# Kernel optimization log

Hardware: AMD Instinct MI355X
Metric: run time of the kernel (lower is better)

## Reference

```python
import jax, jax.numpy as jnp
import numpy as np

B, S, H = 8, 2048, 1024

def setup_inputs() -> dict:
    key = jax.random.key(0)
    k1, k2 = jax.random.split(key)
    inputs = jax.random.normal(k1, (B, S, H), dtype=jnp.float32)
    # PyTorch Linear weight [out, in]; init ~ U(-1/sqrt(H), 1/sqrt(H)) approximated with scaled normal
    W = jax.random.normal(k2, (H, H), dtype=jnp.float32) * (1.0 / np.sqrt(H))
    b = jnp.zeros((H,), dtype=jnp.float32)
    return {"inputs": inputs, "W": W, "b": b}

def reference(inputs, W, b):
    # QW = inputs @ W^T + b   (nn.Linear)
    QW = jnp.einsum('bsh,oh->bso', inputs, W) + b  # [B,S,H]
    # score = QW @ inputs^T  (no scaling, no mask)
    score = jnp.einsum('bqh,bkh->bqk', QW, inputs)  # [B,S,S]
    attn = jax.nn.softmax(score, axis=2)
    # output = attn @ inputs
    output = jnp.einsum('bqk,bkh->bqh', attn, inputs)  # [B,S,H]
    return output
```

## Files before the change

kernel.cpp:

```cpp
#include <hip/hip_runtime.h>
#include <hip/hip_bf16.h>
#include <hip/hip_fp16.h>

typedef unsigned short u16;
typedef __attribute__((ext_vector_type(8))) _Float16 f16x8;
typedef __attribute__((ext_vector_type(4))) float f32x4;

#define B_ 8
#define S_ 2048
#define H_ 1024
#define M_ (B_ * S_)

__device__ __forceinline__ u16 f2h(float f) {
  _Float16 h = (_Float16)f;
  return __builtin_bit_cast(u16, h);
}

__global__ void f32_to_f16_kernel(const float* __restrict__ x,
                                  u16* __restrict__ o, int n4) {
  int stride = gridDim.x * blockDim.x;
  for (int i = blockIdx.x * blockDim.x + threadIdx.x; i < n4; i += stride) {
    float4 v = reinterpret_cast<const float4*>(x)[i];
    ushort4 h;
    h.x = f2h(v.x); h.y = f2h(v.y); h.z = f2h(v.z); h.w = f2h(v.w);
    reinterpret_cast<ushort4*>(o)[i] = h;
  }
}

__global__ __launch_bounds__(256) void transpose_f32_kernel(
    const float* __restrict__ x, u16* __restrict__ xt, u16* __restrict__ xf) {
  __shared__ u16 t[64][72];
  int b = blockIdx.z, s0 = blockIdx.x * 64, h0 = blockIdx.y * 64;
  int tid = threadIdx.x;
  int row = tid & 63, seg = tid >> 6;
  const float* src = x + ((size_t)(b * S_ + s0 + row)) * H_ + h0 + seg * 16;
  u16* dstf = xf + ((size_t)(b * S_ + s0 + row)) * H_ + h0 + seg * 16;
#pragma unroll
  for (int j = 0; j < 4; ++j) {
    float4 v = reinterpret_cast<const float4*>(src)[j];
    ushort4 h;
    h.x = f2h(v.x); h.y = f2h(v.y); h.z = f2h(v.z); h.w = f2h(v.w);
    reinterpret_cast<ushort4*>(dstf)[j] = h;
    *reinterpret_cast<ushort4*>(&t[row][seg * 16 + j * 4]) = h;
  }
  __syncthreads();
  int hh = tid & 63, ss = tid >> 6;
  u16* dst = xt + ((size_t)(b * H_ + h0 + hh)) * S_ + s0 + ss * 16;
#pragma unroll
  for (int j = 0; j < 4; ++j) {
    ushort4 o;
    o.x = t[ss * 16 + j * 4 + 0][hh];
    o.y = t[ss * 16 + j * 4 + 1][hh];
    o.z = t[ss * 16 + j * 4 + 2][hh];
    o.w = t[ss * 16 + j * 4 + 3][hh];
    reinterpret_cast<ushort4*>(dst)[j] = o;
  }
}

__device__ __forceinline__ void async_stage16(const u16* g, u16* l) {
  __builtin_amdgcn_global_load_lds(
      (__attribute__((address_space(1))) void*)g,
      (__attribute__((address_space(3))) void*)l, 16, 0, 0);
}

template <int OM>
__global__ __launch_bounds__(512) void gemm8_kernel(
    const u16* __restrict__ A, const u16* __restrict__ B,
    float* __restrict__ Cf, u16* __restrict__ Ch,
    const float* __restrict__ bias,
    int lda, int ldb, int ldc, int K,
    long sAz, long sBz, long sCz) {
  __shared__ __align__(16) u16 sA[2][256 * 64];
  __shared__ __align__(16) u16 sB[2][256 * 64];

  int gx = gridDim.x, gy = gridDim.y;
  int nwg = gx * gy * gridDim.z;
  int wgid = blockIdx.x + gx * (blockIdx.y + gy * blockIdx.z);
  int q = nwg >> 3, r = nwg & 7;
  int xcd = wgid & 7, idx = wgid >> 3;
  int nid = (xcd < r ? xcd * (q + 1) : r * (q + 1) + (xcd - r) * q) + idx;
  int bxi = nid % gx, t2 = nid / gx;
  int byi = t2 % gy, bzi = t2 / gy;

  int tid = threadIdx.x, wave = tid >> 6, lane = tid & 63;
  int wm = wave >> 2, wn = wave & 3;
  int bm = bxi * 256, bn = byi * 256;
  long zA = (long)bzi * sAz;
  long zB = (long)bzi * sBz;
  long zC = (long)bzi * sCz;
  const u16* gA = A + zA + (size_t)bm * lda;
  const u16* gB = B + zB + (size_t)bn * ldb;

  int srow = tid >> 3;
  int scolb = (tid & 7) << 4;
  int sco = (scolb ^ ((srow & 7) << 4)) >> 1;
  size_t aO0 = (size_t)srow * lda + sco, aO1 = aO0 + (size_t)64 * lda;
  size_t bO0 = (size_t)srow * ldb + sco, bO1 = bO0 + (size_t)64 * ldb;
  int ld0 = srow * 64 + (scolb >> 1), ld1 = ld0 + 64 * 64;

  auto stgA = [&](int slot, int half, int kofs) {
    const u16* g = gA + (size_t)(half * 128) * lda + kofs;
    u16* l = &sA[slot][half * 8192];
    async_stage16(g + aO0, l + ld0);
    async_stage16(g + aO1, l + ld1);
  };
  auto stgB = [&](int slot, int half, int kofs) {
    const u16* g = gB + (size_t)(half * 128) * ldb + kofs;
    u16* l = &sB[slot][half * 8192];
    async_stage16(g + bO0, l + ld0);
    async_stage16(g + bO1, l + ld1);
  };

  int la = lane & 15;
  int kg = (lane >> 4) << 4;
  auto frag = [&](const u16* base, int row, int colb) -> f16x8 {
    int off = (row << 7) + (colb ^ ((row & 7) << 4));
    return *reinterpret_cast<const f16x8*>(
        reinterpret_cast<const char*>(base) + off);
  };

  f16x8 aF0[4][2], aF1[4][2];
  f16x8 bF0[2][2], bF1[2][2];
  f32x4 acc[8][4] = {};

  auto RA = [&](int slot, int qm, f16x8(&dst)[4][2]) {
#pragma unroll
    for (int j = 0; j < 4; ++j)
#pragma unroll
      for (int ks = 0; ks < 2; ++ks)
        dst[j][ks] = frag(sA[slot], qm * 128 + (j * 2 + wm) * 16 + la,
                          ks * 64 + kg);
  };
  auto RB = [&](int slot, int qn, f16x8(&dst)[2][2]) {
#pragma unroll
    for (int i = 0; i < 2; ++i)
#pragma unroll
      for (int ks = 0; ks < 2; ++ks)
        dst[i][ks] = frag(sB[slot], qn * 128 + (i * 4 + wn) * 16 + la,
                          ks * 64 + kg);
  };
  auto MM = [&](int qm, int qn, f16x8(&a)[4][2], f16x8(&b)[2][2]) {
#pragma unroll
    for (int ks = 0; ks < 2; ++ks)
#pragma unroll
      for (int j = 0; j < 4; ++j)
#pragma unroll
        for (int i = 0; i < 2; ++i)
          acc[qm * 4 + j][qn * 2 + i] = __builtin_amdgcn_mfma_f32_16x16x32_f16(
              a[j][ks], b[i][ks], acc[qm * 4 + j][qn * 2 + i], 0, 0, 0);
  };

#define VM6 asm volatile("s_waitcnt vmcnt(6)" ::: "memory")
#define VM0 asm volatile("s_waitcnt vmcnt(0)" ::: "memory")
#define BAR __builtin_amdgcn_s_barrier()
#define PRIO1 __builtin_amdgcn_s_setprio(1)
#define PRIO0 __builtin_amdgcn_s_setprio(0)

  int NT = K >> 6;
  stgA(0, 0, 0); stgB(0, 0, 0); stgB(0, 1, 0); stgA(0, 1, 0);
  if (NT > 1) { stgA(1, 0, 64); stgB(1, 1, 64); stgA(1, 1, 64); }
  VM6;
  BAR;

  for (int t = 0; t < NT; ++t) {
    int s = t & 1, ns = s ^ 1;
    int k1 = (t + 1) << 6, k2 = (t + 2) << 6;
    bool p1 = (t + 1 < NT), p2 = (t + 2 < NT);
    RA(s, 0, aF0); RB(s, 0, bF0);
    RB(s, 1, bF1);
    if (p1) stgB(ns, 0, k1);
    PRIO1; MM(0, 0, aF0, bF0); PRIO0; BAR;
    RA(s, 1, aF1);
    if (p2) stgA(s, 0, k2);
    PRIO1; MM(0, 1, aF0, bF1); PRIO0; BAR;
    if (p2) stgB(s, 1, k2);
    PRIO1; MM(1, 1, aF1, bF1); PRIO0; BAR;
    if (p2) stgA(s, 1, k2);
    PRIO1; MM(1, 0, aF1, bF0); PRIO0;
    if (t < NT - 2) { VM6; } else if (t == NT - 2) { VM0; }
    BAR;
  }
#undef VM6
#undef VM0
#undef BAR
#undef PRIO1
#undef PRIO0

#pragma unroll
  for (int mf = 0; mf < 8; ++mf) {
    int qm = mf >> 2, j = mf & 3;
    int row = bm + qm * 128 + (j * 2 + wm) * 16 + (lane >> 4) * 4;
#pragma unroll
    for (int nf = 0; nf < 4; ++nf) {
      int qn = nf >> 1, i = nf & 1;
      int col = bn + qn * 128 + (i * 4 + wn) * 16 + la;
#pragma unroll
      for (int r = 0; r < 4; ++r) {
        float v = acc[mf][nf][r];
        if constexpr (OM == 1) {
          Ch[zC + (size_t)(row + r) * ldc + col] = f2h(v + bias[col]);
        } else {
          Cf[zC + (size_t)(row + r) * ldc + col] = v;
        }
      }
    }
  }
}

__global__ __launch_bounds__(256) void softmax_kernel(const float* __restrict__ sc,
                                                      u16* __restrict__ attn,
                                                      int opitch) {
  __shared__ float red[4];
  size_t row = blockIdx.x;
  const float* p = sc + row * S_;
  u16* o = attn + row * (size_t)opitch;
  int t = threadIdx.x;
  float4 v0 = reinterpret_cast<const float4*>(p)[t];
  float4 v1 = reinterpret_cast<const float4*>(p)[t + 256];
  float mx = fmaxf(fmaxf(fmaxf(v0.x, v0.y), fmaxf(v0.z, v0.w)),
                   fmaxf(fmaxf(v1.x, v1.y), fmaxf(v1.z, v1.w)));
#pragma unroll
  for (int d = 32; d > 0; d >>= 1) mx = fmaxf(mx, __shfl_xor(mx, d));
  if ((t & 63) == 0) red[t >> 6] = mx;
  __syncthreads();
  mx = fmaxf(fmaxf(red[0], red[1]), fmaxf(red[2], red[3]));
  float e[8];
  e[0] = __expf(v0.x - mx); e[1] = __expf(v0.y - mx);
  e[2] = __expf(v0.z - mx); e[3] = __expf(v0.w - mx);
  e[4] = __expf(v1.x - mx); e[5] = __expf(v1.y - mx);
  e[6] = __expf(v1.z - mx); e[7] = __expf(v1.w - mx);
  float s = ((e[0] + e[1]) + (e[2] + e[3])) + ((e[4] + e[5]) + (e[6] + e[7]));
#pragma unroll
  for (int d = 32; d > 0; d >>= 1) s += __shfl_xor(s, d);
  __syncthreads();
  if ((t & 63) == 0) red[t >> 6] = s;
  __syncthreads();
  s = (red[0] + red[1]) + (red[2] + red[3]);
  float inv = 1.0f / s;
  ushort4 h0, h1;
  h0.x = f2h(e[0] * inv); h0.y = f2h(e[1] * inv);
  h0.z = f2h(e[2] * inv); h0.w = f2h(e[3] * inv);
  h1.x = f2h(e[4] * inv); h1.y = f2h(e[5] * inv);
  h1.z = f2h(e[6] * inv); h1.w = f2h(e[7] * inv);
  reinterpret_cast<ushort4*>(o)[t] = h0;
  reinterpret_cast<ushort4*>(o)[t + 256] = h1;
}

extern "C" void kernel_launch(void* const* d_in, const int* in_sizes, int n_in,
                              void* d_out, int out_size, void* d_ws, size_t ws_size,
                              hipStream_t stream) {
  const float* X = (const float*)d_in[0];
  const float* W = (const float*)d_in[1];
  const float* bias = (const float*)d_in[2];
  float* out = (float*)d_out;
  char* ws = (char*)d_ws;

  const size_t MB = 1ull << 20;
  u16* XF = (u16*)(ws);
  u16* WF = (u16*)(ws + 32 * MB);
  u16* XT = (u16*)(ws + 34 * MB);
  u16* QW = (u16*)(ws + 66 * MB);
  float* SC = (float*)(ws + 98 * MB);

  int CB = (ws_size >= 226 * MB) ? 8 : 4;
  int nch = B_ / CB;

  f32_to_f16_kernel<<<1024, 256, 0, stream>>>(W, WF, H_ * H_ / 4);
  transpose_f32_kernel<<<dim3(S_ / 64, H_ / 64, B_), 256, 0, stream>>>(
      X, XT, XF);
  gemm8_kernel<1><<<dim3(M_ / 256, H_ / 256, 1), 512, 0, stream>>>(
      XF, WF, nullptr, QW, bias, H_, H_, H_, H_, 0, 0, 0);
  for (int ch = 0; ch < nch; ++ch) {
    long off = (long)ch * CB;
    gemm8_kernel<0><<<dim3(S_ / 256, S_ / 256, CB), 512, 0, stream>>>(
        QW + off * S_ * H_, XF + off * S_ * H_, SC, nullptr, nullptr,
        H_, H_, S_, H_, (long)S_ * H_, (long)S_ * H_, (long)S_ * S_);
    softmax_kernel<<<CB * S_, 256, 0, stream>>>(SC, (u16*)SC, 2 * S_);
    gemm8_kernel<0><<<dim3(S_ / 256, H_ / 256, CB), 512, 0, stream>>>(
        (u16*)SC, XT + off * (long)H_ * S_,
        out + off * (long)S_ * H_, nullptr, nullptr,
        2 * S_, S_, H_, S_, (long)S_ * 2 * S_, (long)H_ * S_, (long)S_ * H_);
  }
}
```

Measured before the change: 257.5 us.

## Shrink GEMM tiles to 128x256 with BK=32 and new LDS swizzle

New measurement: 302.8 us. 17.6% more time.

```diff
diff --git a/kernel.cpp b/kernel.cpp
--- a/kernel.cpp
+++ b/kernel.cpp
@@ -70,8 +70,8 @@
     const float* __restrict__ bias,
     int lda, int ldb, int ldc, int K,
     long sAz, long sBz, long sCz) {
-  __shared__ __align__(16) u16 sA[2][256 * 64];
-  __shared__ __align__(16) u16 sB[2][256 * 64];
+  __shared__ __align__(16) u16 sA[2][4096];
+  __shared__ __align__(16) u16 sB[2][8192];
 
   int gx = gridDim.x, gy = gridDim.y;
   int nwg = gx * gy * gridDim.z;
@@ -84,123 +84,109 @@
 
   int tid = threadIdx.x, wave = tid >> 6, lane = tid & 63;
   int wm = wave >> 2, wn = wave & 3;
-  int bm = bxi * 256, bn = byi * 256;
+  int bm = bxi * 128, bn = byi * 256;
   long zA = (long)bzi * sAz;
   long zB = (long)bzi * sBz;
   long zC = (long)bzi * sCz;
   const u16* gA = A + zA + (size_t)bm * lda;
   const u16* gB = B + zB + (size_t)bn * ldb;
 
-  int srow = tid >> 3;
-  int scolb = (tid & 7) << 4;
-  int sco = (scolb ^ ((srow & 7) << 4)) >> 1;
-  size_t aO0 = (size_t)srow * lda + sco, aO1 = aO0 + (size_t)64 * lda;
-  size_t bO0 = (size_t)srow * ldb + sco, bO1 = bO0 + (size_t)64 * ldb;
-  int ld0 = srow * 64 + (scolb >> 1), ld1 = ld0 + 64 * 64;
-
-  auto stgA = [&](int slot, int half, int kofs) {
-    const u16* g = gA + (size_t)(half * 128) * lda + kofs;
-    u16* l = &sA[slot][half * 8192];
-    async_stage16(g + aO0, l + ld0);
-    async_stage16(g + aO1, l + ld1);
+  int cS = (tid & 3) ^ ((tid >> 3) & 3);
+  int rowB = ((tid >> 6) << 4) + ((tid & 63) >> 2);
+  int rowA = (((tid & 255) >> 6) << 4) + ((tid & 63) >> 2);
+  int halfA = tid >> 8;
+  size_t aOff = (size_t)(halfA * 64 + rowA) * lda + cS * 8;
+  size_t bOff = (size_t)rowB * ldb + cS * 8;
+  int dstOff = tid * 8;
+
+  auto stgA = [&](int slot, int kofs) {
+    async_stage16(gA + aOff + kofs, &sA[slot][0] + dstOff);
   };
   auto stgB = [&](int slot, int half, int kofs) {
-    const u16* g = gB + (size_t)(half * 128) * ldb + kofs;
-    u16* l = &sB[slot][half * 8192];
-    async_stage16(g + bO0, l + ld0);
-    async_stage16(g + bO1, l + ld1);
+    async_stage16(gB + (size_t)half * 128 * ldb + bOff + kofs,
+                  &sB[slot][half * 4096] + dstOff);
   };
 
   int la = lane & 15;
-  int kg = (lane >> 4) << 4;
-  auto frag = [&](const u16* base, int row, int colb) -> f16x8 {
-    int off = (row << 7) + (colb ^ ((row & 7) << 4));
+  int kq = lane >> 4;
+  auto frag = [&](const u16* base, int row) -> f16x8 {
+    int off = ((row >> 4) << 10) + ((row & 15) << 6) +
+              ((kq ^ ((row >> 1) & 3)) << 4);
     return *reinterpret_cast<const f16x8*>(
         reinterpret_cast<const char*>(base) + off);
   };
 
-  f16x8 aF0[4][2], aF1[4][2];
-  f16x8 bF0[2][2], bF1[2][2];
-  f32x4 acc[8][4] = {};
-
-  auto RA = [&](int slot, int qm, f16x8(&dst)[4][2]) {
-#pragma unroll
-    for (int j = 0; j < 4; ++j)
-#pragma unroll
-      for (int ks = 0; ks < 2; ++ks)
-        dst[j][ks] = frag(sA[slot], qm * 128 + (j * 2 + wm) * 16 + la,
-                          ks * 64 + kg);
-  };
-  auto RB = [&](int slot, int qn, f16x8(&dst)[2][2]) {
+  f16x8 aF0[2], aF1[2], bF0[2], bF1[2];
+  f32x4 acc[4][4] = {};
+
+  auto RA = [&](int slot, int qm, f16x8(&dst)[2]) {
+#pragma unroll
+    for (int j = 0; j < 2; ++j)
+      dst[j] = frag(&sA[slot][qm * 2048], (j * 2 + wm) * 16 + la);
+  };
+  auto RB = [&](int slot, int qn, f16x8(&dst)[2]) {
 #pragma unroll
     for (int i = 0; i < 2; ++i)
-#pragma unroll
-      for (int ks = 0; ks < 2; ++ks)
-        dst[i][ks] = frag(sB[slot], qn * 128 + (i * 4 + wn) * 16 + la,
-                          ks * 64 + kg);
-  };
-  auto MM = [&](int qm, int qn, f16x8(&a)[4][2], f16x8(&b)[2][2]) {
-#pragma unroll
-    for (int ks = 0; ks < 2; ++ks)
-#pragma unroll
-      for (int j = 0; j < 4; ++j)
-#pragma unroll
-        for (int i = 0; i < 2; ++i)
-          acc[qm * 4 + j][qn * 2 + i] = __builtin_amdgcn_mfma_f32_16x16x32_f16(
-              a[j][ks], b[i][ks], acc[qm * 4 + j][qn * 2 + i], 0, 0, 0);
-  };
-
-#define VM6 asm volatile("s_waitcnt vmcnt(6)" ::: "memory")
+      dst[i] = frag(&sB[slot][qn * 4096], (i * 4 + wn) * 16 + la);
+  };
+  auto MM = [&](int qm, int qn, f16x8(&a)[2], f16x8(&b)[2]) {
+#pragma unroll
+    for (int j = 0; j < 2; ++j)
+#pragma unroll
+      for (int i = 0; i < 2; ++i)
+        acc[qm * 2 + j][qn * 2 + i] = __builtin_amdgcn_mfma_f32_16x16x32_f16(
+            a[j], b[i], acc[qm * 2 + j][qn * 2 + i], 0, 0, 0);
+  };
+
+#define VM2 asm volatile("s_waitcnt vmcnt(2)" ::: "memory")
 #define VM0 asm volatile("s_waitcnt vmcnt(0)" ::: "memory")
 #define BAR __builtin_amdgcn_s_barrier()
 #define PRIO1 __builtin_amdgcn_s_setprio(1)
 #define PRIO0 __builtin_amdgcn_s_setprio(0)
 
-  int NT = K >> 6;
-  stgA(0, 0, 0); stgB(0, 0, 0); stgB(0, 1, 0); stgA(0, 1, 0);
-  if (NT > 1) { stgA(1, 0, 64); stgB(1, 1, 64); stgA(1, 1, 64); }
-  VM6;
+  int NT = K >> 5;
+  stgB(0, 0, 0); stgB(0, 1, 0); stgA(0, 0);
+  if (NT > 1) { stgB(1, 1, 32); stgA(1, 32); }
+  VM2;
   BAR;
 
   for (int t = 0; t < NT; ++t) {
     int s = t & 1, ns = s ^ 1;
-    int k1 = (t + 1) << 6, k2 = (t + 2) << 6;
+    int k1 = (t + 1) << 5, k2 = (t + 2) << 5;
     bool p1 = (t + 1 < NT), p2 = (t + 2 < NT);
-    RA(s, 0, aF0); RB(s, 0, bF0);
-    RB(s, 1, bF1);
+    RA(s, 0, aF0); RB(s, 0, bF0); RB(s, 1, bF1);
     if (p1) stgB(ns, 0, k1);
     PRIO1; MM(0, 0, aF0, bF0); PRIO0; BAR;
     RA(s, 1, aF1);
-    if (p2) stgA(s, 0, k2);
     PRIO1; MM(0, 1, aF0, bF1); PRIO0; BAR;
     if (p2) stgB(s, 1, k2);
     PRIO1; MM(1, 1, aF1, bF1); PRIO0; BAR;
-    if (p2) stgA(s, 1, k2);
+    if (p2) stgA(s, k2);
     PRIO1; MM(1, 0, aF1, bF0); PRIO0;
-    if (t < NT - 2) { VM6; } else if (t == NT - 2) { VM0; }
+    if (t < NT - 2) { VM2; } else if (t == NT - 2) { VM0; }
     BAR;
   }
-#undef VM6
+#undef VM2
 #undef VM0
 #undef BAR
 #undef PRIO1
 #undef PRIO0
 
 #pragma unroll
-  for (int mf = 0; mf < 8; ++mf) {
-    int qm = mf >> 2, j = mf & 3;
-    int row = bm + qm * 128 + (j * 2 + wm) * 16 + (lane >> 4) * 4;
-#pragma unroll
-    for (int nf = 0; nf < 4; ++nf) {
-      int qn = nf >> 1, i = nf & 1;
+  for (int mi = 0; mi < 4; ++mi) {
+    int qm = mi >> 1, j = mi & 1;
+    int rowb = bm + qm * 64 + (j * 2 + wm) * 16 + (lane >> 4) * 4;
+#pragma unroll
+    for (int ni = 0; ni < 4; ++ni) {
+      int qn = ni >> 1, i = ni & 1;
       int col = bn + qn * 128 + (i * 4 + wn) * 16 + la;
 #pragma unroll
       for (int r = 0; r < 4; ++r) {
-        float v = acc[mf][nf][r];
+        float v = acc[mi][ni][r];
         if constexpr (OM == 1) {
-          Ch[zC + (size_t)(row + r) * ldc + col] = f2h(v + bias[col]);
+          Ch[zC + (size_t)(rowb + r) * ldc + col] = f2h(v + bias[col]);
         } else {
-          Cf[zC + (size_t)(row + r) * ldc + col] = v;
+          Cf[zC + (size_t)(rowb + r) * ldc + col] = v;
         }
       }
     }
@@ -262,21 +248,21 @@
   u16* QW = (u16*)(ws + 66 * MB);
   float* SC = (float*)(ws + 98 * MB);
 
-  int CB = (ws_size >= 226 * MB) ? 8 : 4;
+  int CB = (ws_size >= 163 * MB) ? 4 : 2;
   int nch = B_ / CB;
 
   f32_to_f16_kernel<<<1024, 256, 0, stream>>>(W, WF, H_ * H_ / 4);
   transpose_f32_kernel<<<dim3(S_ / 64, H_ / 64, B_), 256, 0, stream>>>(
       X, XT, XF);
-  gemm8_kernel<1><<<dim3(M_ / 256, H_ / 256, 1), 512, 0, stream>>>(
+  gemm8_kernel<1><<<dim3(M_ / 128, H_ / 256, 1), 512, 0, stream>>>(
       XF, WF, nullptr, QW, bias, H_, H_, H_, H_, 0, 0, 0);
   for (int ch = 0; ch < nch; ++ch) {
     long off = (long)ch * CB;
-    gemm8_kernel<0><<<dim3(S_ / 256, S_ / 256, CB), 512, 0, stream>>>(
+    gemm8_kernel<0><<<dim3(S_ / 128, S_ / 256, CB), 512, 0, stream>>>(
         QW + off * S_ * H_, XF + off * S_ * H_, SC, nullptr, nullptr,
         H_, H_, S_, H_, (long)S_ * H_, (long)S_ * H_, (long)S_ * S_);
     softmax_kernel<<<CB * S_, 256, 0, stream>>>(SC, (u16*)SC, 2 * S_);
-    gemm8_kernel<0><<<dim3(S_ / 256, H_ / 256, CB), 512, 0, stream>>>(
+    gemm8_kernel<0><<<dim3(S_ / 128, H_ / 256, CB), 512, 0, stream>>>(
         (u16*)SC, XT + off * (long)H_ * S_,
         out + off * (long)S_ * H_, nullptr, nullptr,
         2 * S_, S_, H_, S_, (long)S_ * 2 * S_, (long)H_ * S_, (long)S_ * H_);
```

## Add 256x128 GEMM tile variant for attn@V and shrink batch chunk size

Applied to the files above, without the earlier changes.

After: 268.6 us. 1.04x slower.

```diff
diff --git a/kernel.cpp b/kernel.cpp
--- a/kernel.cpp
+++ b/kernel.cpp
@@ -63,7 +63,7 @@
       (__attribute__((address_space(3))) void*)l, 16, 0, 0);
 }
 
-template <int OM>
+template <int OM, int NB>
 __global__ __launch_bounds__(512) void gemm8_kernel(
     const u16* __restrict__ A, const u16* __restrict__ B,
     float* __restrict__ Cf, u16* __restrict__ Ch,
@@ -71,7 +71,7 @@
     int lda, int ldb, int ldc, int K,
     long sAz, long sBz, long sCz) {
   __shared__ __align__(16) u16 sA[2][256 * 64];
-  __shared__ __align__(16) u16 sB[2][256 * 64];
+  __shared__ __align__(16) u16 sB[2][NB * 128 * 64];
 
   int gx = gridDim.x, gy = gridDim.y;
   int nwg = gx * gy * gridDim.z;
@@ -84,7 +84,7 @@
 
   int tid = threadIdx.x, wave = tid >> 6, lane = tid & 63;
   int wm = wave >> 2, wn = wave & 3;
-  int bm = bxi * 256, bn = byi * 256;
+  int bm = bxi * 256, bn = byi * (NB * 128);
   long zA = (long)bzi * sAz;
   long zB = (long)bzi * sBz;
   long zC = (long)bzi * sCz;
@@ -121,7 +121,7 @@
 
   f16x8 aF0[4][2], aF1[4][2];
   f16x8 bF0[2][2], bF1[2][2];
-  f32x4 acc[8][4] = {};
+  f32x4 acc[8][NB * 2] = {};
 
   auto RA = [&](int slot, int qm, f16x8(&dst)[4][2]) {
 #pragma unroll
@@ -151,36 +151,58 @@
   };
 
 #define VM6 asm volatile("s_waitcnt vmcnt(6)" ::: "memory")
+#define VM4 asm volatile("s_waitcnt vmcnt(4)" ::: "memory")
 #define VM0 asm volatile("s_waitcnt vmcnt(0)" ::: "memory")
 #define BAR __builtin_amdgcn_s_barrier()
 #define PRIO1 __builtin_amdgcn_s_setprio(1)
 #define PRIO0 __builtin_amdgcn_s_setprio(0)
 
   int NT = K >> 6;
-  stgA(0, 0, 0); stgB(0, 0, 0); stgB(0, 1, 0); stgA(0, 1, 0);
-  if (NT > 1) { stgA(1, 0, 64); stgB(1, 1, 64); stgA(1, 1, 64); }
-  VM6;
-  BAR;
-
-  for (int t = 0; t < NT; ++t) {
-    int s = t & 1, ns = s ^ 1;
-    int k1 = (t + 1) << 6, k2 = (t + 2) << 6;
-    bool p1 = (t + 1 < NT), p2 = (t + 2 < NT);
-    RA(s, 0, aF0); RB(s, 0, bF0);
-    RB(s, 1, bF1);
-    if (p1) stgB(ns, 0, k1);
-    PRIO1; MM(0, 0, aF0, bF0); PRIO0; BAR;
-    RA(s, 1, aF1);
-    if (p2) stgA(s, 0, k2);
-    PRIO1; MM(0, 1, aF0, bF1); PRIO0; BAR;
-    if (p2) stgB(s, 1, k2);
-    PRIO1; MM(1, 1, aF1, bF1); PRIO0; BAR;
-    if (p2) stgA(s, 1, k2);
-    PRIO1; MM(1, 0, aF1, bF0); PRIO0;
-    if (t < NT - 2) { VM6; } else if (t == NT - 2) { VM0; }
+
+  if constexpr (NB == 2) {
+    stgA(0, 0, 0); stgB(0, 0, 0); stgB(0, 1, 0); stgA(0, 1, 0);
+    if (NT > 1) { stgA(1, 0, 64); stgB(1, 1, 64); stgA(1, 1, 64); }
+    VM6;
     BAR;
+    for (int t = 0; t < NT; ++t) {
+      int s = t & 1, ns = s ^ 1;
+      int k1 = (t + 1) << 6, k2 = (t + 2) << 6;
+      bool p1 = (t + 1 < NT), p2 = (t + 2 < NT);
+      RA(s, 0, aF0); RB(s, 0, bF0);
+      RB(s, 1, bF1);
+      if (p1) stgB(ns, 0, k1);
+      PRIO1; MM(0, 0, aF0, bF0); PRIO0; BAR;
+      RA(s, 1, aF1);
+      if (p2) stgA(s, 0, k2);
+      PRIO1; MM(0, 1, aF0, bF1); PRIO0; BAR;
+      if (p2) stgB(s, 1, k2);
+      PRIO1; MM(1, 1, aF1, bF1); PRIO0; BAR;
+      if (p2) stgA(s, 1, k2);
+      PRIO1; MM(1, 0, aF1, bF0); PRIO0;
+      if (t < NT - 2) { VM6; } else if (t == NT - 2) { VM0; }
+      BAR;
+    }
+  } else {
+    stgB(0, 0, 0); stgA(0, 0, 0); stgA(0, 1, 0);
+    if (NT > 1) { stgB(1, 0, 64); stgA(1, 0, 64); }
+    VM4;
+    BAR;
+    for (int t = 0; t < NT; ++t) {
+      int s = t & 1, ns = s ^ 1;
+      int k1 = (t + 1) << 6, k2 = (t + 2) << 6;
+      bool p1 = (t + 1 < NT), p2 = (t + 2 < NT);
+      RA(s, 0, aF0); RB(s, 0, bF0);
+      RA(s, 1, aF1);
+      if (p1) stgA(ns, 1, k1);
+      PRIO1; MM(0, 0, aF0, bF0); PRIO0; BAR;
+      if (p2) { stgB(s, 0, k2); stgA(s, 0, k2); }
+      PRIO1; MM(1, 0, aF1, bF0); PRIO0;
+      if (t < NT - 2) { VM4; } else if (t == NT - 2) { VM0; }
+      BAR;
+    }
   }
 #undef VM6
+#undef VM4
 #undef VM0
 #undef BAR
 #undef PRIO1
@@ -191,7 +213,7 @@
     int qm = mf >> 2, j = mf & 3;
     int row = bm + qm * 128 + (j * 2 + wm) * 16 + (lane >> 4) * 4;
 #pragma unroll
-    for (int nf = 0; nf < 4; ++nf) {
+    for (int nf = 0; nf < NB * 2; ++nf) {
       int qn = nf >> 1, i = nf & 1;
       int col = bn + qn * 128 + (i * 4 + wn) * 16 + la;
 #pragma unroll
@@ -262,21 +284,21 @@
   u16* QW = (u16*)(ws + 66 * MB);
   float* SC = (float*)(ws + 98 * MB);
 
-  int CB = (ws_size >= 226 * MB) ? 8 : 4;
+  int CB = (ws_size >= 163 * MB) ? 4 : 2;
   int nch = B_ / CB;
 
   f32_to_f16_kernel<<<1024, 256, 0, stream>>>(W, WF, H_ * H_ / 4);
   transpose_f32_kernel<<<dim3(S_ / 64, H_ / 64, B_), 256, 0, stream>>>(
       X, XT, XF);
-  gemm8_kernel<1><<<dim3(M_ / 256, H_ / 256, 1), 512, 0, stream>>>(
+  gemm8_kernel<1, 2><<<dim3(M_ / 256, H_ / 256, 1), 512, 0, stream>>>(
       XF, WF, nullptr, QW, bias, H_, H_, H_, H_, 0, 0, 0);
   for (int ch = 0; ch < nch; ++ch) {
     long off = (long)ch * CB;
-    gemm8_kernel<0><<<dim3(S_ / 256, S_ / 256, CB), 512, 0, stream>>>(
+    gemm8_kernel<0, 2><<<dim3(S_ / 256, S_ / 256, CB), 512, 0, stream>>>(
         QW + off * S_ * H_, XF + off * S_ * H_, SC, nullptr, nullptr,
         H_, H_, S_, H_, (long)S_ * H_, (long)S_ * H_, (long)S_ * S_);
     softmax_kernel<<<CB * S_, 256, 0, stream>>>(SC, (u16*)SC, 2 * S_);
-    gemm8_kernel<0><<<dim3(S_ / 256, H_ / 256, CB), 512, 0, stream>>>(
+    gemm8_kernel<0, 1><<<dim3(S_ / 256, H_ / 128, CB), 512, 0, stream>>>(
         (u16*)SC, XT + off * (long)H_ * S_,
         out + off * (long)S_ * H_, nullptr, nullptr,
         2 * S_, S_, H_, S_, (long)S_ * 2 * S_, (long)H_ * S_, (long)S_ * H_);
```
